# Performance work log

Measured on AMD Instinct MI355X. Metric: run time of the kernel, lower is better.

The kernel has to match this reference:

```python
import jax, jax.numpy as jnp
import numpy as np

B_, H_, W_ = 4, 64, 64
D_MODEL, D_INNER, N_STATE, R_RANK, K_ = 96, 192, 16, 6, 4
EPS = 1e-5

def silu(v):
    return v * jax.nn.sigmoid(v)

def setup_inputs() -> dict:
    key = jax.random.key(0)
    ks = jax.random.split(key, 8)
    d, dm = D_INNER, D_MODEL
    A = jnp.tile(jnp.arange(1, N_STATE + 1, dtype=jnp.float32)[None, :], (K_ * d, 1))
    return {
        "x": jax.random.normal(ks[0], (B_, H_, W_, dm), jnp.float32),
        "in_proj_w": jax.random.normal(ks[1], (2 * d, dm), jnp.float32) * 0.02,
        "conv_w": jax.random.normal(ks[2], (d, 1, 3, 3), jnp.float32) * 0.1,
        "conv_b": jnp.zeros((d,), jnp.float32),
        "x_proj_weight": jax.random.normal(ks[3], (K_, R_RANK + 2 * N_STATE, d), jnp.float32) * 0.05,
        "dt_projs_weight": jax.random.normal(ks[4], (K_, d, R_RANK), jnp.float32) * 0.1,
        "dt_projs_bias": jax.random.normal(ks[5], (K_, d), jnp.float32) * 0.1,
        "A_logs": jnp.log(A),
        "Ds": jnp.ones((K_ * d,), jnp.float32),
        "out_norm_w": jnp.ones((d,), jnp.float32),
        "out_norm_b": jnp.zeros((d,), jnp.float32),
        "out_proj_w": jax.random.normal(ks[6], (dm, d), jnp.float32) * 0.02,
    }

def selective_scan(u, dts, As, Bs, Cs, Ds, dt_bias):
    # u, dts: [B,K,D,L]; As: [K,D,N]; Bs, Cs: [B,K,N,L]; Ds, dt_bias: [K,D]
    delta = jax.nn.softplus(dts + dt_bias[None, :, :, None])
    dT = jnp.moveaxis(delta, -1, 0)  # [L,B,K,D]
    uT = jnp.moveaxis(u, -1, 0)      # [L,B,K,D]
    BT = jnp.moveaxis(Bs, -1, 0)     # [L,B,K,N]
    CT = jnp.moveaxis(Cs, -1, 0)     # [L,B,K,N]
    h0 = jnp.zeros((u.shape[0], K_, D_INNER, N_STATE), jnp.float32)

    def step(h, inps):
        dt, ut, bt, ct = inps
        h = jnp.exp(dt[..., None] * As[None]) * h + (dt * ut)[..., None] * bt[:, :, None, :]
        y = jnp.einsum('bkdn,bkn->bkd', h, ct)
        return h, y

    _, ys = jax.lax.scan(step, h0, (dT, uT, BT, CT))
    ys = jnp.moveaxis(ys, 0, -1)  # [B,K,D,L]
    return ys + u * Ds[None, :, :, None]

def reference(x, in_proj_w, conv_w, conv_b, x_proj_weight, dt_projs_weight,
              dt_projs_bias, A_logs, Ds, out_norm_w, out_norm_b, out_proj_w):
    B, H, W, dm = x.shape
    d, N, R, K = D_INNER, N_STATE, R_RANK, K_
    L = H * W
    # in_proj + z gate (SiLU)
    xz = jnp.einsum('bhwc,pc->bhwp', x, in_proj_w)  # [B,H,W,2d]
    xc, z = xz[..., :d], xz[..., d:]
    z = silu(z)
    # depthwise conv (NCHW) + SiLU
    xc = jnp.transpose(xc, (0, 3, 1, 2))  # [B,d,H,W]
    xc = jax.lax.conv_general_dilated(
        xc, conv_w, (1, 1), 'SAME', feature_group_count=d,
        dimension_numbers=('NCHW', 'OIHW', 'NCHW')) + conv_b[None, :, None, None]
    xc = silu(xc)
    # cross-scan: 4 directions
    x0 = xc.reshape(B, d, L)                                   # row-major
    x1 = jnp.transpose(xc, (0, 1, 3, 2)).reshape(B, d, L)       # col-major
    xs = jnp.stack([x0, x1, x0[..., ::-1], x1[..., ::-1]], axis=1)  # [B,K,D,L]
    # projections
    x_dbl = jnp.einsum('bkdl,kcd->bkcl', xs, x_proj_weight)
    dts, Bs, Cs = jnp.split(x_dbl, [R, R + N], axis=2)
    dts = jnp.einsum('bkrl,kdr->bkdl', dts, dt_projs_weight)
    As = -jnp.exp(A_logs).reshape(K, d, N)
    ys = selective_scan(xs, dts, As, Bs, Cs, Ds.reshape(K, d), dt_projs_bias)
    # cross-merge
    y_wh = (ys[:, 1] + ys[:, 3, :, ::-1]).reshape(B, d, W, H)
    y_wh = jnp.transpose(y_wh, (0, 1, 3, 2)).reshape(B, d, L)
    y = ys[:, 0] + ys[:, 2, :, ::-1] + y_wh                     # [B,d,L]
    y = jnp.transpose(y.reshape(B, d, H, W), (0, 2, 3, 1))       # [B,H,W,d]
    # out_norm: LayerNorm over channel dim
    mu = jnp.mean(y, axis=-1, keepdims=True)
    var = jnp.mean((y - mu) ** 2, axis=-1, keepdims=True)
    y = out_norm_w * (y - mu) * jax.lax.rsqrt(var + EPS) + out_norm_b
    # gate + out_proj
    y = y * z
    return jnp.einsum('bhwd,cd->bhwc', y, out_proj_w)
```

## Files before the change

### kernel.cpp

```cpp
#include <hip/hip_runtime.h>
#include <math.h>

#define B_ 4
#define HH 64
#define WW 64
#define LL 4096
#define DM 96
#define DI 192
#define NS 16
#define RR 6
#define KK 4
#define NROW (B_ * KK * DI)
#define XPS 160
#define KOFF 40
#define DPT 3

__device__ __forceinline__ int pix_of(int k, int l) {
    switch (k) {
        case 0: return l;
        case 1: { int w = l >> 6, h = l & 63; return (h << 6) + w; }
        case 2: return (LL - 1) - l;
        default: { int ll = (LL - 1) - l; int w = ll >> 6, h = ll & 63; return (h << 6) + w; }
    }
}

__device__ __forceinline__ float silu_f(float v) {
    return v * __fdividef(1.f, 1.f + __expf(-v));
}
__device__ __forceinline__ float softplus_f(float x) {
    return (x > 20.f) ? x : __logf(1.f + __expf(x));
}

template<int MODE>
__global__ __launch_bounds__(256)
void gemm_kernel(const float* __restrict__ A, const float* __restrict__ Bw,
                 float* __restrict__ C0, float* __restrict__ C1,
                 int M, int N, int Kd) {
    __shared__ float As[32][68];
    __shared__ float Bs[32][68];
    int tid = threadIdx.x;
    int tx = tid & 15, ty = tid >> 4;
    int m0 = blockIdx.y * 64, n0 = blockIdx.x * 64;
    float acc[4][4] = {};
    for (int k0 = 0; k0 < Kd; k0 += 32) {
        #pragma unroll
        for (int i = 0; i < 8; ++i) {
            int idx = tid + i * 256;
            int r = idx >> 5, c = idx & 31;
            As[c][r] = A[(size_t)(m0 + r) * Kd + k0 + c];
            int rn = n0 + r;
            Bs[c][r] = (rn < N) ? Bw[(size_t)rn * Kd + k0 + c] : 0.f;
        }
        __syncthreads();
        #pragma unroll
        for (int kk = 0; kk < 32; ++kk) {
            float4 av = *(const float4*)&As[kk][ty * 4];
            float4 bv = *(const float4*)&Bs[kk][tx * 4];
            const float* avp = (const float*)&av;
            const float* bvp = (const float*)&bv;
            #pragma unroll
            for (int i = 0; i < 4; ++i)
                #pragma unroll
                for (int j = 0; j < 4; ++j)
                    acc[i][j] += avp[i] * bvp[j];
        }
        __syncthreads();
    }
    #pragma unroll
    for (int i = 0; i < 4; ++i) {
        int m = m0 + ty * 4 + i;
        #pragma unroll
        for (int j = 0; j < 4; ++j) {
            int n = n0 + tx * 4 + j;
            if (n >= N) continue;
            float v = acc[i][j];
            if (MODE == 0) {
                if (n < DI) C0[(size_t)m * DI + n] = v;
                else        C1[(size_t)m * DI + (n - DI)] = silu_f(v);
            } else if (MODE == 1) {
                C0[(size_t)m * N + n] = v;
            } else {
                if (n < 152) {
                    int kd = n / 38, c = n - kd * 38;
                    C0[(size_t)m * XPS + kd * KOFF + c] = v;
                }
            }
        }
    }
}

__global__ __launch_bounds__(192)
void conv_kernel(const float* __restrict__ xc, const float* __restrict__ cw,
                 const float* __restrict__ cb, float* __restrict__ out) {
    int p0 = blockIdx.x * 8;
    int b = blockIdx.y;
    int c = threadIdx.x;
    int h = p0 >> 6, w0 = p0 & 63;
    float kw[9];
    #pragma unroll
    for (int j = 0; j < 9; ++j) kw[j] = cw[c * 9 + j];
    float xv[3][10];
    #pragma unroll
    for (int dh = 0; dh < 3; ++dh) {
        int hh = h + dh - 1;
        bool hv = (hh >= 0 && hh < HH);
        #pragma unroll
        for (int j = 0; j < 10; ++j) {
            int ww = w0 + j - 1;
            bool v = hv && (ww >= 0 && ww < WW);
            xv[dh][j] = v ? xc[((size_t)(b << 12) + (hh << 6) + ww) * DI + c] : 0.f;
        }
    }
    float bias = cb[c];
    #pragma unroll
    for (int w = 0; w < 8; ++w) {
        float acc = bias;
        #pragma unroll
        for (int dh = 0; dh < 3; ++dh)
            #pragma unroll
            for (int dc = 0; dc < 3; ++dc)
                acc += xv[dh][w + dc] * kw[dh * 3 + dc];
        out[((size_t)(b << 12) + p0 + w) * DI + c] = silu_f(acc);
    }
}

template<int PHASE, int NCHT>
__global__ __launch_bounds__(64)
void scan_phase(const float* __restrict__ xconv, const float* __restrict__ xdblP,
                const float* __restrict__ dtw, const float* __restrict__ dtb,
                const float* __restrict__ A_logs, const float* __restrict__ Ds,
                float* __restrict__ carryA, float* __restrict__ carryB,
                float* __restrict__ y_acc) {
    constexpr int CHL = LL / NCHT;
    constexpr int NV4 = (PHASE == 3) ? (KOFF / 4) : 6;
    int chunk = blockIdx.x;
    int k = blockIdx.y;
    int b = blockIdx.z;
    int lane = threadIdx.x;
    int l0 = chunk * CHL;
    __shared__ float sx[CHL * NV4 * 4];
    float4* sx4 = (float4*)sx;
    const float* xb = xdblP + ((size_t)(b << 12)) * XPS + k * KOFF;
    for (int idx = lane; idx < CHL * NV4; idx += 64) {
        int r = idx / NV4, j = idx - r * NV4;
        int p = pix_of(k, l0 + r);
        sx4[idx] = *(const float4*)(xb + (size_t)p * XPS + j * 4);
    }

    float wr[DPT][RR], bias[DPT], Dk[DPT], sumDelta[DPT];
    float h[DPT][NS];
    const float* alog[DPT];
    bool fastA = true;
    #pragma unroll
    for (int j = 0; j < DPT; ++j) {
        int d = lane + 64 * j;
        #pragma unroll
        for (int r = 0; r < RR; ++r) wr[j][r] = dtw[(k * DI + d) * RR + r];
        bias[j] = dtb[k * DI + d];
        alog[j] = A_logs + (size_t)(k * DI + d) * NS;
        #pragma unroll
        for (int n = 0; n < NS; ++n) {
            float an = -__expf(alog[j][n]);
            fastA = fastA && (fabsf(an + (float)(n + 1)) < 1e-4f * (float)(n + 1));
        }
        int row = (b * KK + k) * DI + d;
        if (PHASE == 1) {
            #pragma unroll
            for (int n = 0; n < NS; ++n) h[j][n] = 0.f;
        } else {
            const float4* cb4 = (const float4*)(carryB + ((size_t)chunk * NROW + row) * NS);
            #pragma unroll
            for (int q = 0; q < NS / 4; ++q) {
                float4 v = cb4[q];
                h[j][q * 4 + 0] = v.x; h[j][q * 4 + 1] = v.y;
                h[j][q * 4 + 2] = v.z; h[j][q * 4 + 3] = v.w;
            }
        }
        Dk[j] = (PHASE == 3) ? Ds[k * DI + d] : 0.f;
        sumDelta[j] = 0.f;
    }
    const float* ubase = xconv + (size_t)(b << 12) * DI + lane;
    float* ybase = y_acc + (size_t)(b << 12) * DI + lane;
    __syncthreads();

    int p_cur = pix_of(k, l0);
    float u_cur[DPT];
    #pragma unroll
    for (int j = 0; j < DPT; ++j) u_cur[j] = ubase[(size_t)p_cur * DI + 64 * j];
    for (int i = 0; i < CHL; ++i) {
        int p_nxt = 0;
        float u_nxt[DPT] = {};
        if (i + 1 < CHL) {
            p_nxt = pix_of(k, l0 + i + 1);
            #pragma unroll
            for (int j = 0; j < DPT; ++j) u_nxt[j] = ubase[(size_t)p_nxt * DI + 64 * j];
        }
        float xrv[NV4 * 4];
        float4* x4 = (float4*)xrv;
        #pragma unroll
        for (int j = 0; j < NV4; ++j) x4[j] = sx4[i * NV4 + j];
        #pragma unroll
        for (int j = 0; j < DPT; ++j) {
            float dtraw = bias[j];
            #pragma unroll
            for (int r = 0; r < RR; ++r) dtraw += xrv[r] * wr[j][r];
            float delta = softplus_f(dtraw);
            if (PHASE == 1) sumDelta[j] += delta;
            float du = delta * u_cur[j];
            float y = 0.f;
            if (fastA) {
                float g = __expf(-delta);
                float a = 1.f;
                #pragma unroll
                for (int n = 0; n < NS; ++n) {
                    a *= g;
                    h[j][n] = a * h[j][n] + du * xrv[6 + n];
                    if (PHASE == 3) y += h[j][n] * xrv[22 + n];
                }
            } else {
                #pragma unroll
                for (int n = 0; n < NS; ++n) {
                    float a = __expf(delta * (-__expf(alog[j][n])));
                    h[j][n] = a * h[j][n] + du * xrv[6 + n];
                    if (PHASE == 3) y += h[j][n] * xrv[22 + n];
                }
            }
            if (PHASE == 3) {
                y += u_cur[j] * Dk[j];
                atomicAdd(&ybase[(size_t)p_cur * DI + 64 * j], y);
            }
        }
        p_cur = p_nxt;
        #pragma unroll
        for (int j = 0; j < DPT; ++j) u_cur[j] = u_nxt[j];
    }
    if (PHASE == 1) {
        #pragma unroll
        for (int j = 0; j < DPT; ++j) {
            int row = (b * KK + k) * DI + lane + 64 * j;
            float4* ca4 = (float4*)(carryA + ((size_t)chunk * NROW + row) * NS);
            float4* cb4 = (float4*)(carryB + ((size_t)chunk * NROW + row) * NS);
            #pragma unroll
            for (int q = 0; q < NS / 4; ++q) {
                float4 va, vb;
                va.x = __expf(-__expf(alog[j][q * 4 + 0]) * sumDelta[j]);
                va.y = __expf(-__expf(alog[j][q * 4 + 1]) * sumDelta[j]);
                va.z = __expf(-__expf(alog[j][q * 4 + 2]) * sumDelta[j]);
                va.w = __expf(-__expf(alog[j][q * 4 + 3]) * sumDelta[j]);
                vb.x = h[j][q * 4 + 0]; vb.y = h[j][q * 4 + 1];
                vb.z = h[j][q * 4 + 2]; vb.w = h[j][q * 4 + 3];
                ca4[q] = va;
                cb4[q] = vb;
            }
        }
    }
}

template<int NCHT>
__global__ __launch_bounds__(256)
void scan_chunks(const float* __restrict__ carryA, float* __restrict__ carryB) {
    int t = blockIdx.x * 256 + threadIdx.x;
    if (t >= NROW * NS) return;
    float h = 0.f;
    for (int c = 0; c < NCHT; ++c) {
        size_t idx = (size_t)c * (NROW * NS) + t;
        float a = carryA[idx], bb = carryB[idx];
        carryB[idx] = h;
        h = a * h + bb;
    }
}

__global__ __launch_bounds__(256)
void ln_kernel(const float* __restrict__ y_acc, const float* __restrict__ z_silu,
               const float* __restrict__ nw, const float* __restrict__ nb,
               float* __restrict__ out) {
    int pg = blockIdx.x * 4 + (threadIdx.x >> 6);
    int lane = threadIdx.x & 63;
    const float* yr = y_acc + (size_t)pg * DI;
    float v0 = yr[lane], v1 = yr[lane + 64], v2 = yr[lane + 128];
    float s = v0 + v1 + v2;
    float sq = v0 * v0 + v1 * v1 + v2 * v2;
    #pragma unroll
    for (int m = 32; m >= 1; m >>= 1) {
        s  += __shfl_xor(s, m, 64);
        sq += __shfl_xor(sq, m, 64);
    }
    float mu = s * (1.f / 192.f);
    float var = sq * (1.f / 192.f) - mu * mu;
    float rs = rsqrtf(var + 1e-5f);
    const float* zr = z_silu + (size_t)pg * DI;
    float* o = out + (size_t)pg * DI;
    float vv[3] = {v0, v1, v2};
    #pragma unroll
    for (int j = 0; j < 3; ++j) {
        int c = lane + j * 64;
        o[c] = (nw[c] * (vv[j] - mu) * rs + nb[c]) * zr[c];
    }
}

extern "C" void kernel_launch(void* const* d_in, const int* in_sizes, int n_in,
                              void* d_out, int out_size, void* d_ws, size_t ws_size,
                              hipStream_t stream) {
    const float* x        = (const float*)d_in[0];
    const float* in_projw = (const float*)d_in[1];
    const float* conv_w   = (const float*)d_in[2];
    const float* conv_b   = (const float*)d_in[3];
    const float* x_projw  = (const float*)d_in[4];
    const float* dt_w     = (const float*)d_in[5];
    const float* dt_b     = (const float*)d_in[6];
    const float* A_logs   = (const float*)d_in[7];
    const float* Ds       = (const float*)d_in[8];
    const float* nw       = (const float*)d_in[9];
    const float* nb       = (const float*)d_in[10];
    const float* opw      = (const float*)d_in[11];
    float* out = (float*)d_out;
    float* ws = (float*)d_ws;

    const size_t SZ = (size_t)B_ * LL * DI;
    const size_t XD = (size_t)B_ * LL * XPS;

    const size_t car128 = (size_t)NROW * 128 * NS;
    const size_t need128 = (3 * SZ + XD + 2 * car128) * sizeof(float);
    bool big = (ws_size >= need128);

    float* z_silu = ws;
    float* xc_raw = ws + SZ;
    float* xconv  = ws + 2 * SZ;
    float* xdblP  = ws + 3 * SZ;
    float* carryA = ws + 3 * SZ + XD;
    float* carryB = carryA + (big ? car128 : (size_t)NROW * 64 * NS);
    float* y_acc  = xc_raw;
    float* yln    = xconv;

    gemm_kernel<0><<<dim3(6, 256), 256, 0, stream>>>(x, in_projw, xc_raw, z_silu,
                                                     B_ * LL, 2 * DI, DM);
    conv_kernel<<<dim3(LL / 8, B_), DI, 0, stream>>>(xc_raw, conv_w, conv_b, xconv);
    gemm_kernel<2><<<dim3(3, 256), 256, 0, stream>>>(xconv, x_projw, xdblP, nullptr,
                                                     B_ * LL, 152, DI);

    if (big) {
        scan_phase<1, 128><<<dim3(128, KK, B_), 64, 0, stream>>>(xconv, xdblP, dt_w, dt_b,
                                                                 A_logs, Ds, carryA, carryB, nullptr);
        scan_chunks<128><<<(NROW * NS + 255) / 256, 256, 0, stream>>>(carryA, carryB);
        hipMemsetAsync(y_acc, 0, SZ * sizeof(float), stream);
        scan_phase<3, 128><<<dim3(128, KK, B_), 64, 0, stream>>>(xconv, xdblP, dt_w, dt_b,
                                                                 A_logs, Ds, carryA, carryB, y_acc);
    } else {
        scan_phase<1, 64><<<dim3(64, KK, B_), 64, 0, stream>>>(xconv, xdblP, dt_w, dt_b,
                                                               A_logs, Ds, carryA, carryB, nullptr);
        scan_chunks<64><<<(NROW * NS + 255) / 256, 256, 0, stream>>>(carryA, carryB);
        hipMemsetAsync(y_acc, 0, SZ * sizeof(float), stream);
        scan_phase<3, 64><<<dim3(64, KK, B_), 64, 0, stream>>>(xconv, xdblP, dt_w, dt_b,
                                                               A_logs, Ds, carryA, carryB, y_acc);
    }
    ln_kernel<<<(B_ * LL) / 4, 256, 0, stream>>>(y_acc, z_silu, nw, nb, yln);
    gemm_kernel<1><<<dim3(2, 256), 256, 0, stream>>>(yln, opw, out, nullptr,
                                                     B_ * LL, DM, DI);
}
```

Baseline: 224.9 us.

## Store per-chunk delta sums instead of carryA, double scan chunks, hoist A check

Phase 1 now writes one summed delta per row instead of a full 16-wide carryA decay tensor. scan_chunks recomputes the decay from A_logs and that sum, which cuts carry storage and traffic roughly in half and lets the chunk count double from 128 to 256 for more parallelism. The per-thread fastA check moves into a separate prep kernel that sets a global flag, and pixel indexing becomes pointer increments by a fixed stride. In exchange there are two extra launches (a memset and prep_kernel), more exp work in the chunk scan, and a longer sequential carry chain.

```diff
diff --git a/kernel.cpp b/kernel.cpp
--- a/kernel.cpp
+++ b/kernel.cpp
@@ -124,13 +124,22 @@
     }
 }
 
+__global__ __launch_bounds__(256)
+void prep_kernel(const float* __restrict__ A_logs, int* __restrict__ flag) {
+    int t = blockIdx.x * 256 + threadIdx.x;
+    if (t >= KK * DI * NS) return;
+    int n = t & 15;
+    float an = -__expf(A_logs[t]);
+    if (!(fabsf(an + (float)(n + 1)) < 1e-4f * (float)(n + 1))) atomicOr(flag, 1);
+}
+
 template<int PHASE, int NCHT>
 __global__ __launch_bounds__(64)
 void scan_phase(const float* __restrict__ xconv, const float* __restrict__ xdblP,
                 const float* __restrict__ dtw, const float* __restrict__ dtb,
                 const float* __restrict__ A_logs, const float* __restrict__ Ds,
-                float* __restrict__ carryA, float* __restrict__ carryB,
-                float* __restrict__ y_acc) {
+                float* __restrict__ sumD, float* __restrict__ carryB,
+                float* __restrict__ y_acc, const int* __restrict__ flag) {
     constexpr int CHL = LL / NCHT;
     constexpr int NV4 = (PHASE == 3) ? (KOFF / 4) : 6;
     int chunk = blockIdx.x;
@@ -150,7 +159,7 @@
     float wr[DPT][RR], bias[DPT], Dk[DPT], sumDelta[DPT];
     float h[DPT][NS];
     const float* alog[DPT];
-    bool fastA = true;
+    bool fastA = (*flag == 0);
     #pragma unroll
     for (int j = 0; j < DPT; ++j) {
         int d = lane + 64 * j;
@@ -158,11 +167,6 @@
         for (int r = 0; r < RR; ++r) wr[j][r] = dtw[(k * DI + d) * RR + r];
         bias[j] = dtb[k * DI + d];
         alog[j] = A_logs + (size_t)(k * DI + d) * NS;
-        #pragma unroll
-        for (int n = 0; n < NS; ++n) {
-            float an = -__expf(alog[j][n]);
-            fastA = fastA && (fabsf(an + (float)(n + 1)) < 1e-4f * (float)(n + 1));
-        }
         int row = (b * KK + k) * DI + d;
         if (PHASE == 1) {
             #pragma unroll
@@ -179,21 +183,22 @@
         Dk[j] = (PHASE == 3) ? Ds[k * DI + d] : 0.f;
         sumDelta[j] = 0.f;
     }
-    const float* ubase = xconv + (size_t)(b << 12) * DI + lane;
-    float* ybase = y_acc + (size_t)(b << 12) * DI + lane;
     __syncthreads();
 
-    int p_cur = pix_of(k, l0);
+    int s = (k == 0) ? 1 : (k == 1) ? 64 : (k == 2) ? -1 : -64;
+    int p0 = pix_of(k, l0);
+    intptr_t stp = (intptr_t)s * DI;
+    const float* up = xconv + (size_t)(b << 12) * DI + (size_t)p0 * DI + lane;
+    float* yp = y_acc + (size_t)(b << 12) * DI + (size_t)p0 * DI + lane;
     float u_cur[DPT];
     #pragma unroll
-    for (int j = 0; j < DPT; ++j) u_cur[j] = ubase[(size_t)p_cur * DI + 64 * j];
+    for (int j = 0; j < DPT; ++j) u_cur[j] = up[64 * j];
+
     for (int i = 0; i < CHL; ++i) {
-        int p_nxt = 0;
         float u_nxt[DPT] = {};
         if (i + 1 < CHL) {
-            p_nxt = pix_of(k, l0 + i + 1);
-            #pragma unroll
-            for (int j = 0; j < DPT; ++j) u_nxt[j] = ubase[(size_t)p_nxt * DI + 64 * j];
+            #pragma unroll
+            for (int j = 0; j < DPT; ++j) u_nxt[j] = up[stp + 64 * j];
         }
         float xrv[NV4 * 4];
         float4* x4 = (float4*)xrv;
@@ -227,10 +232,11 @@
             }
             if (PHASE == 3) {
                 y += u_cur[j] * Dk[j];
-                atomicAdd(&ybase[(size_t)p_cur * DI + 64 * j], y);
-            }
-        }
-        p_cur = p_nxt;
+                atomicAdd(yp + 64 * j, y);
+            }
+        }
+        if (PHASE == 3) yp += stp;
+        up += stp;
         #pragma unroll
         for (int j = 0; j < DPT; ++j) u_cur[j] = u_nxt[j];
     }
@@ -238,34 +244,35 @@
         #pragma unroll
         for (int j = 0; j < DPT; ++j) {
             int row = (b * KK + k) * DI + lane + 64 * j;
-            float4* ca4 = (float4*)(carryA + ((size_t)chunk * NROW + row) * NS);
             float4* cb4 = (float4*)(carryB + ((size_t)chunk * NROW + row) * NS);
             #pragma unroll
             for (int q = 0; q < NS / 4; ++q) {
-                float4 va, vb;
-                va.x = __expf(-__expf(alog[j][q * 4 + 0]) * sumDelta[j]);
-                va.y = __expf(-__expf(alog[j][q * 4 + 1]) * sumDelta[j]);
-                va.z = __expf(-__expf(alog[j][q * 4 + 2]) * sumDelta[j]);
-                va.w = __expf(-__expf(alog[j][q * 4 + 3]) * sumDelta[j]);
+                float4 vb;
                 vb.x = h[j][q * 4 + 0]; vb.y = h[j][q * 4 + 1];
                 vb.z = h[j][q * 4 + 2]; vb.w = h[j][q * 4 + 3];
-                ca4[q] = va;
                 cb4[q] = vb;
             }
+            sumD[(size_t)chunk * NROW + row] = sumDelta[j];
         }
     }
 }
 
 template<int NCHT>
 __global__ __launch_bounds__(256)
-void scan_chunks(const float* __restrict__ carryA, float* __restrict__ carryB) {
+void scan_chunks(const float* __restrict__ sumD, const float* __restrict__ A_logs,
+                 float* __restrict__ carryB) {
     int t = blockIdx.x * 256 + threadIdx.x;
     if (t >= NROW * NS) return;
+    int row = t >> 4, n = t & 15;
+    int kd = row % (KK * DI);
+    float An = -__expf(A_logs[(size_t)kd * NS + n]);
     float h = 0.f;
+    #pragma unroll 4
     for (int c = 0; c < NCHT; ++c) {
         size_t idx = (size_t)c * (NROW * NS) + t;
-        float a = carryA[idx], bb = carryB[idx];
+        float bb = carryB[idx];
         carryB[idx] = h;
+        float a = __expf(An * sumD[(size_t)c * NROW + row]);
         h = a * h + bb;
     }
 }
@@ -318,40 +325,43 @@
 
     const size_t SZ = (size_t)B_ * LL * DI;
     const size_t XD = (size_t)B_ * LL * XPS;
-
-    const size_t car128 = (size_t)NROW * 128 * NS;
-    const size_t need128 = (3 * SZ + XD + 2 * car128) * sizeof(float);
-    bool big = (ws_size >= need128);
+    const size_t CAR256 = (size_t)NROW * 256 * NS;
+    const size_t CAR128 = (size_t)NROW * 128 * NS;
+    const size_t need256 = (3 * SZ + XD + CAR256 + (size_t)NROW * 256 + 16) * sizeof(float);
+    bool big = (ws_size >= need256);
 
     float* z_silu = ws;
     float* xc_raw = ws + SZ;
     float* xconv  = ws + 2 * SZ;
     float* xdblP  = ws + 3 * SZ;
-    float* carryA = ws + 3 * SZ + XD;
-    float* carryB = carryA + (big ? car128 : (size_t)NROW * 64 * NS);
+    float* carryB = ws + 3 * SZ + XD;
+    float* sumD   = carryB + (big ? CAR256 : CAR128);
+    int*   flag   = (int*)(sumD + (size_t)NROW * (big ? 256 : 128));
     float* y_acc  = xc_raw;
     float* yln    = xconv;
 
     gemm_kernel<0><<<dim3(6, 256), 256, 0, stream>>>(x, in_projw, xc_raw, z_silu,
                                                      B_ * LL, 2 * DI, DM);
+    hipMemsetAsync(flag, 0, sizeof(int), stream);
+    prep_kernel<<<(KK * DI * NS + 255) / 256, 256, 0, stream>>>(A_logs, flag);
     conv_kernel<<<dim3(LL / 8, B_), DI, 0, stream>>>(xc_raw, conv_w, conv_b, xconv);
     gemm_kernel<2><<<dim3(3, 256), 256, 0, stream>>>(xconv, x_projw, xdblP, nullptr,
                                                      B_ * LL, 152, DI);
 
     if (big) {
+        scan_phase<1, 256><<<dim3(256, KK, B_), 64, 0, stream>>>(xconv, xdblP, dt_w, dt_b,
+                                                                 A_logs, Ds, sumD, carryB, nullptr, flag);
+        scan_chunks<256><<<(NROW * NS + 255) / 256, 256, 0, stream>>>(sumD, A_logs, carryB);
+        hipMemsetAsync(y_acc, 0, SZ * sizeof(float), stream);
+        scan_phase<3, 256><<<dim3(256, KK, B_), 64, 0, stream>>>(xconv, xdblP, dt_w, dt_b,
+                                                                 A_logs, Ds, sumD, carryB, y_acc, flag);
+    } else {
         scan_phase<1, 128><<<dim3(128, KK, B_), 64, 0, stream>>>(xconv, xdblP, dt_w, dt_b,
-                                                                 A_logs, Ds, carryA, carryB, nullptr);
-        scan_chunks<128><<<(NROW * NS + 255) / 256, 256, 0, stream>>>(carryA, carryB);
+                                                                 A_logs, Ds, sumD, carryB, nullptr, flag);
+        scan_chunks<128><<<(NROW * NS + 255) / 256, 256, 0, stream>>>(sumD, A_logs, carryB);
         hipMemsetAsync(y_acc, 0, SZ * sizeof(float), stream);
         scan_phase<3, 128><<<dim3(128, KK, B_), 64, 0, stream>>>(xconv, xdblP, dt_w, dt_b,
-                                                                 A_logs, Ds, carryA, carryB, y_acc);
-    } else {
-        scan_phase<1, 64><<<dim3(64, KK, B_), 64, 0, stream>>>(xconv, xdblP, dt_w, dt_b,
-                                                               A_logs, Ds, carryA, carryB, nullptr);
-        scan_chunks<64><<<(NROW * NS + 255) / 256, 256, 0, stream>>>(carryA, carryB);
-        hipMemsetAsync(y_acc, 0, SZ * sizeof(float), stream);
-        scan_phase<3, 64><<<dim3(64, KK, B_), 64, 0, stream>>>(xconv, xdblP, dt_w, dt_b,
-                                                               A_logs, Ds, carryA, carryB, y_acc);
+                                                                 A_logs, Ds, sumD, carryB, y_acc, flag);
     }
     ln_kernel<<<(B_ * LL) / 4, 256, 0, stream>>>(y_acc, z_silu, nw, nb, yln);
     gemm_kernel<1><<<dim3(2, 256), 256, 0, stream>>>(yln, opw, out, nullptr,
```

Measured after the change: 245.1 us. 1.09x slower.
